# Performance work log

Hardware: AMD Instinct MI355X
Metric: run time of the kernel (lower is better)

Reference implementation:

```python
import jax, jax.numpy as jnp
import numpy as np

B, S, F = 16, 128, 64          # batch, seq_len, feature_dim
H = 256                        # hidden_dim
HEADS = 4
DH = H // HEADS                # GAT per-head dim = 64
AH = (2 * H) // HEADS          # temporal-attn head dim = 128
N = 1024                       # num graph nodes (edge_index.max()+1)
E = 16384                      # num edges (avg degree 16)
D2 = 2 * H                     # bi-LSTM output dim = 512
BN_INV = 1.0 / np.sqrt(1.0 + 1e-5)   # eval-mode BatchNorm1d (running mean=0, var=1)


def lstm_dir(x_sf, Wih, Whh, bih, bhh):
    # x_sf: [S, B, F]; torch gate order i, f, g, o
    h0 = jnp.zeros((x_sf.shape[1], Whh.shape[1]), x_sf.dtype)
    def step(carry, xt):
        h, c = carry
        z = xt @ Wih.T + h @ Whh.T + bih + bhh
        i, f, g, o = jnp.split(z, 4, axis=-1)
        c = jax.nn.sigmoid(f) * c + jax.nn.sigmoid(i) * jnp.tanh(g)
        h = jax.nn.sigmoid(o) * jnp.tanh(c)
        return (h, c), h
    _, hs = jax.lax.scan(step, (h0, h0), x_sf)
    return hs


def setup_inputs():
    key = jax.random.key(0)
    ks = jax.random.split(key, 32)
    g = lambda i, sh: jax.random.normal(ks[i], sh, jnp.float32) * 0.05
    return {
        "x": jax.random.normal(ks[0], (B, S, F), jnp.float32),
        "edge_index": jax.random.randint(ks[1], (2, E), 0, N),
        "Wih_f": g(2, (4 * H, F)), "Whh_f": g(3, (4 * H, H)),
        "bih_f": g(4, (4 * H,)), "bhh_f": g(5, (4 * H,)),
        "Wih_b": g(6, (4 * H, F)), "Whh_b": g(7, (4 * H, H)),
        "bih_b": g(8, (4 * H,)), "bhh_b": g(9, (4 * H,)),
        "Wq": g(10, (D2, D2)), "bq": g(11, (D2,)),
        "Wk": g(12, (D2, D2)), "bk": g(13, (D2,)),
        "Wv": g(14, (D2, D2)), "bv": g(15, (D2,)),
        "Wo": g(16, (D2, D2)), "bo": g(17, (D2,)),
        "W1": g(18, (D2, H)), "a1s": g(19, (HEADS, DH)), "a1d": g(20, (HEADS, DH)), "b1": g(21, (H,)),
        "g1": jnp.ones((H,), jnp.float32), "be1": jnp.zeros((H,), jnp.float32),
        "W2": g(22, (H, H)), "a2s": g(23, (HEADS, DH)), "a2d": g(24, (HEADS, DH)), "b2": g(25, (H,)),
        "g2": jnp.ones((H,), jnp.float32), "be2": jnp.zeros((H,), jnp.float32),
        "Wf": g(26, (H, 3 * H)), "bf": g(27, (H,)),
        "ln_g": jnp.ones((H,), jnp.float32), "ln_b": jnp.zeros((H,), jnp.float32),
    }


def reference(x, edge_index, Wih_f, Whh_f, bih_f, bhh_f, Wih_b, Whh_b, bih_b, bhh_b,
              Wq, bq, Wk, bk, Wv, bv, Wo, bo,
              W1, a1s, a1d, b1, g1, be1, W2, a2s, a2d, b2, g2, be2,
              Wf, bf, ln_g, ln_b):
    # ---- bidirectional LSTM ----
    xs = jnp.swapaxes(x, 0, 1)                                   # [S,B,F]
    hf = lstm_dir(xs, Wih_f, Whh_f, bih_f, bhh_f)
    hb = jnp.flip(lstm_dir(jnp.flip(xs, 0), Wih_b, Whh_b, bih_b, bhh_b), 0)
    t = jnp.swapaxes(jnp.concatenate([hf, hb], -1), 0, 1)        # [B,S,2H]
    # ---- temporal multi-head attention ----
    def proj(W, b):
        return (t @ W.T + b).reshape(B, S, HEADS, AH).transpose(0, 2, 1, 3)
    Q, K, V = proj(Wq, bq), proj(Wk, bk), proj(Wv, bv)
    scores = jnp.einsum('bhqd,bhkd->bhqk', Q, K) / np.sqrt(AH)
    attn = jax.nn.softmax(scores, -1)                            # [B,HEADS,S,S]
    ao = jnp.einsum('bhqk,bhkd->bhqd', attn, V).transpose(0, 2, 1, 3).reshape(B, S, D2)
    last = (ao @ Wo.T + bo)[:, -1, :]                            # [B,2H]
    # ---- 2-layer GAT per sample (PyG GATConv, add_self_loops=True), vmapped over batch ----
    loops = jnp.arange(N)
    src = jnp.concatenate([edge_index[0], loops])
    dst = jnp.concatenate([edge_index[1], loops])
    def gat(h_in, W, a_s, a_d, b):
        h = (h_in @ W).reshape(N, HEADS, DH)
        e = jax.nn.leaky_relu((h * a_s).sum(-1)[src] + (h * a_d).sum(-1)[dst], 0.2)  # [Etot,HEADS]
        m = jax.ops.segment_max(e, dst, num_segments=N)
        w = jnp.exp(e - m[dst])
        z = jax.ops.segment_sum(w, dst, num_segments=N)
        alpha = w / (z[dst] + 1e-16)
        out = jax.ops.segment_sum(alpha[:, :, None] * h[src], dst, num_segments=N)
        return out.reshape(N, H) + b
    def spatial(v):
        feat = jnp.broadcast_to(v, (N, D2))                      # uniform node features, per original
        h1 = jax.nn.elu(gat(feat, W1, a1s, a1d, b1) * BN_INV * g1 + be1)
        h2 = jax.nn.elu(gat(h1, W2, a2s, a2d, b2) * BN_INV * g2 + be2)
        return h2.mean(0)
    sp = jax.vmap(spatial)(last)                                 # [B,H]
    # ---- fusion: Linear + LayerNorm + ReLU (dropout = eval no-op) ----
    f = jnp.concatenate([last, sp], -1) @ Wf.T + bf
    mu = f.mean(-1, keepdims=True)
    var = ((f - mu) ** 2).mean(-1, keepdims=True)
    fused = jax.nn.relu((f - mu) / jnp.sqrt(var + 1e-5) * ln_g + ln_b)
    return fused, attn
```

## Files before the change

### kernel.cpp

```cpp
#include <hip/hip_runtime.h>


typedef unsigned short u16;
typedef unsigned int u32;
typedef __bf16 bf16x8 __attribute__((ext_vector_type(8)));
typedef float f32x4 __attribute__((ext_vector_type(4)));
typedef unsigned short ushort8v __attribute__((ext_vector_type(8)));
typedef unsigned int uint4v __attribute__((ext_vector_type(4)));

#define BN_INV_F 0.9999950000374997f
#define POISON 0xFFFFFFFFu

__device__ __forceinline__ float b2f(u16 u) {
  union { float f; unsigned int i; } v;
  v.i = ((unsigned int)u) << 16;
  return v.f;
}
__device__ __forceinline__ u16 f2b(float f) {
  union { float f; unsigned int i; } v;
  v.f = f;
  unsigned int x = v.i;
  unsigned int r = (x + 0x7FFFu + ((x >> 16) & 1u)) >> 16;
  return (u16)r;
}
__device__ __forceinline__ f32x4 mfma16(ushort8v a, ushort8v b, f32x4 c) {
  return __builtin_amdgcn_mfma_f32_16x16x32_bf16(
      __builtin_bit_cast(bf16x8, a), __builtin_bit_cast(bf16x8, b), c, 0, 0, 0);
}
__device__ __forceinline__ float sigm(float x) { return 1.f / (1.f + __expf(-x)); }
__device__ __forceinline__ float tanh_f(float x) {
  float e = __expf(2.f * x);
  return 1.f - 2.f / (e + 1.f);
}

__global__ __launch_bounds__(256) void lstm_kernel(
    const float* __restrict__ x,
    const float* __restrict__ Wih0, const float* __restrict__ Whh0,
    const float* __restrict__ bih0, const float* __restrict__ bhh0,
    const float* __restrict__ Wih1, const float* __restrict__ Whh1,
    const float* __restrict__ bih1, const float* __restrict__ bhh1,
    u32* __restrict__ hbuf,
    u16* __restrict__ tb)
{
  const int tid = threadIdx.x;
  const int bx = blockIdx.x;
  const int d = bx >> 4;
  const int q = bx & 15;
  const float* Wih = d ? Wih1 : Wih0;
  const float* Whh = d ? Whh1 : Whh0;
  const float* bih = d ? bih1 : bih0;
  const float* bhh = d ? bhh1 : bhh0;

  __shared__ u16 whh_s[64][264];
  __shared__ u16 wih_s[64][72];
  __shared__ u16 h_s[16][264];
  __shared__ u16 x_s[16][72];
  __shared__ float z_s[4][16][17];
  __shared__ float bias_s[64];

  {
    int r = tid >> 2, seg = tid & 3;
    int grow = ((r >> 4) << 8) + q * 16 + (r & 15);
    const float4* src = (const float4*)(Whh + grow * 256 + seg * 64);
#pragma unroll
    for (int i = 0; i < 16; i++) {
      float4 v = src[i];
      whh_s[r][seg * 64 + i * 4 + 0] = f2b(v.x);
      whh_s[r][seg * 64 + i * 4 + 1] = f2b(v.y);
      whh_s[r][seg * 64 + i * 4 + 2] = f2b(v.z);
      whh_s[r][seg * 64 + i * 4 + 3] = f2b(v.w);
    }
    const float4* src2 = (const float4*)(Wih + grow * 64 + seg * 16);
#pragma unroll
    for (int i = 0; i < 4; i++) {
      float4 v = src2[i];
      wih_s[r][seg * 16 + i * 4 + 0] = f2b(v.x);
      wih_s[r][seg * 16 + i * 4 + 1] = f2b(v.y);
      wih_s[r][seg * 16 + i * 4 + 2] = f2b(v.z);
      wih_s[r][seg * 16 + i * 4 + 3] = f2b(v.w);
    }
  }
  if (tid < 64) {
    int grow = ((tid >> 4) << 8) + q * 16 + (tid & 15);
    bias_s[tid] = bih[grow] + bhh[grow];
  }

  const int w = tid >> 6;
  const int ln = tid & 63;
  const int col16 = ln & 15;
  const int quad = ln >> 4;
  const int eb = tid >> 4;
  const int ec = tid & 15;
  float c_reg = 0.f;

  for (int t = 0; t < 128; t++) {
    const int pos = d ? (127 - t) : t;
    {
      int b_ = tid >> 4;
      int f0 = (tid & 15) * 4;
      float4 xv = *(const float4*)(x + (b_ * 128 + pos) * 64 + f0);
      x_s[b_][f0 + 0] = f2b(xv.x);
      x_s[b_][f0 + 1] = f2b(xv.y);
      x_s[b_][f0 + 2] = f2b(xv.z);
      x_s[b_][f0 + 3] = f2b(xv.w);
    }
    if (t > 0) {
      const u32* hw = hbuf + (t * 2 + d) * 2048 + tid * 8;
      uint4v a, b;
      for (;;) {
        asm volatile(
            "global_load_dwordx4 %0, %2, off sc1\n\t"
            "global_load_dwordx4 %1, %3, off sc1\n\t"
            "s_waitcnt vmcnt(0)"
            : "=v"(a), "=v"(b)
            : "v"(hw), "v"(hw + 4)
            : "memory");
        bool ok = (a.x != POISON) & (a.y != POISON) & (a.z != POISON) &
                  (a.w != POISON) & (b.x != POISON) & (b.y != POISON) &
                  (b.z != POISON) & (b.w != POISON);
        if (ok) break;
      }
      int b_ = tid >> 4, c0 = (tid & 15) * 16;
      *(u32*)&h_s[b_][c0 + 0] = a.x;
      *(u32*)&h_s[b_][c0 + 2] = a.y;
      *(u32*)&h_s[b_][c0 + 4] = a.z;
      *(u32*)&h_s[b_][c0 + 6] = a.w;
      *(u32*)&h_s[b_][c0 + 8] = b.x;
      *(u32*)&h_s[b_][c0 + 10] = b.y;
      *(u32*)&h_s[b_][c0 + 12] = b.z;
      *(u32*)&h_s[b_][c0 + 14] = b.w;
    }
    __syncthreads();

    f32x4 acc = {0.f, 0.f, 0.f, 0.f};
#pragma unroll
    for (int kt = 0; kt < 2; kt++) {
      ushort8v av = *(const ushort8v*)&x_s[col16][kt * 32 + quad * 8];
      ushort8v bv = *(const ushort8v*)&wih_s[w * 16 + col16][kt * 32 + quad * 8];
      acc = mfma16(av, bv, acc);
    }
    if (t > 0) {
#pragma unroll
      for (int kt = 0; kt < 8; kt++) {
        ushort8v av = *(const ushort8v*)&h_s[col16][kt * 32 + quad * 8];
        ushort8v bv = *(const ushort8v*)&whh_s[w * 16 + col16][kt * 32 + quad * 8];
        acc = mfma16(av, bv, acc);
      }
    }
#pragma unroll
    for (int reg = 0; reg < 4; reg++)
      z_s[w][quad * 4 + reg][col16] = acc[reg];
    __syncthreads();

    float zi = z_s[0][eb][ec] + bias_s[ec];
    float zf = z_s[1][eb][ec] + bias_s[16 + ec];
    float zg = z_s[2][eb][ec] + bias_s[32 + ec];
    float zo = z_s[3][eb][ec] + bias_s[48 + ec];
    float si = sigm(zi), sf = sigm(zf), so = sigm(zo);
    float tg = tanh_f(zg);
    c_reg = sf * c_reg + si * tg;
    float hv = so * tanh_f(c_reg);
    u32 my = (u32)f2b(hv);
    u32 hi = __shfl_down((int)my, 1);
    if ((ec & 1) == 0) {
      u32 word = my | (hi << 16);
      *(u32*)&tb[(eb * 128 + pos) * 512 + d * 256 + q * 16 + ec] = word;
      if (t < 127) {
        u32* dst = hbuf + ((t + 1) * 2 + d) * 2048 + eb * 128 + (q * 16 + ec) / 2;
        __hip_atomic_store(dst, word, __ATOMIC_RELAXED,
                           __HIP_MEMORY_SCOPE_AGENT);
      }
    }
  }
}

__global__ __launch_bounds__(256) void qkv_kernel(
    const u16* __restrict__ tb,
    const float* __restrict__ Wq, const float* __restrict__ bq,
    const float* __restrict__ Wk, const float* __restrict__ bk,
    const float* __restrict__ Wv, const float* __restrict__ bv,
    u16* __restrict__ Qb, u16* __restrict__ Kb, u16* __restrict__ Vb)
{
  const int tid = threadIdx.x;
  const int bxm = blockIdx.x, byn = blockIdx.y, bz = blockIdx.z;
  const float* W = (bz == 0) ? Wq : ((bz == 1) ? Wk : Wv);
  const float* bias = (bz == 0) ? bq : ((bz == 1) ? bk : bv);
  u16* outp = (bz == 0) ? Qb : ((bz == 1) ? Kb : Vb);

  __shared__ u16 a_s[64][40];
  __shared__ u16 b_s[64][40];
  const int w = tid >> 6, ln = tid & 63, col16 = ln & 15, quad = ln >> 4;

  f32x4 acc[4];
#pragma unroll
  for (int n = 0; n < 4; n++) acc[n] = (f32x4){0.f, 0.f, 0.f, 0.f};

  for (int kt = 0; kt < 16; kt++) {
    int r = tid >> 2, seg = tid & 3;
    *(ushort8v*)&a_s[r][seg * 8] =
        *(const ushort8v*)(tb + (bxm * 64 + r) * 512 + kt * 32 + seg * 8);
    const float4* wsrc = (const float4*)(W + (byn * 64 + r) * 512 + kt * 32 + seg * 8);
    float4 w0 = wsrc[0], w1 = wsrc[1];
    b_s[r][seg * 8 + 0] = f2b(w0.x);
    b_s[r][seg * 8 + 1] = f2b(w0.y);
    b_s[r][seg * 8 + 2] = f2b(w0.z);
    b_s[r][seg * 8 + 3] = f2b(w0.w);
    b_s[r][seg * 8 + 4] = f2b(w1.x);
    b_s[r][seg * 8 + 5] = f2b(w1.y);
    b_s[r][seg * 8 + 6] = f2b(w1.z);
    b_s[r][seg * 8 + 7] = f2b(w1.w);
    __syncthreads();
    ushort8v av = *(const ushort8v*)&a_s[w * 16 + col16][quad * 8];
#pragma unroll
    for (int n = 0; n < 4; n++) {
      ushort8v bvv = *(const ushort8v*)&b_s[n * 16 + col16][quad * 8];
      acc[n] = mfma16(av, bvv, acc[n]);
    }
    __syncthreads();
  }
#pragma unroll
  for (int n = 0; n < 4; n++) {
    float bs = bias[byn * 64 + n * 16 + col16];
#pragma unroll
    for (int reg = 0; reg < 4; reg++) {
      int row = bxm * 64 + w * 16 + quad * 4 + reg;
      outp[row * 512 + byn * 64 + n * 16 + col16] = f2b(acc[n][reg] + bs);
    }
  }
}

__global__ __launch_bounds__(256) void attn_kernel(
    const u16* __restrict__ Qb, const u16* __restrict__ Kb,
    float* __restrict__ attn_out)
{
  const int b = blockIdx.x, h = blockIdx.y, half = blockIdx.z;
  const int tid = threadIdx.x;
  __shared__ __align__(16) char smem[52224];
  u16 (*q_s)[136] = (u16(*)[136])smem;
  u16 (*k_s)[136] = (u16(*)[136])(smem + 17408);
  float (*sc)[132] = (float(*)[132])smem;

  const int w = tid >> 6, ln = tid & 63, col16 = ln & 15, quad = ln >> 4;
  {
    int r = tid >> 2, seg = tid & 3;
    const u16* src = Qb + (b * 128 + half * 64 + r) * 512 + h * 128 + seg * 32;
#pragma unroll
    for (int i = 0; i < 4; i++)
      *(ushort8v*)&q_s[r][seg * 32 + i * 8] = *(const ushort8v*)(src + i * 8);
    int r2 = tid >> 1, sg = tid & 1;
    const u16* src2 = Kb + (b * 128 + r2) * 512 + h * 128 + sg * 64;
#pragma unroll
    for (int i = 0; i < 8; i++)
      *(ushort8v*)&k_s[r2][sg * 64 + i * 8] = *(const ushort8v*)(src2 + i * 8);
  }
  __syncthreads();

  f32x4 acc[8];
#pragma unroll
  for (int n = 0; n < 8; n++) acc[n] = (f32x4){0.f, 0.f, 0.f, 0.f};
#pragma unroll
  for (int kd = 0; kd < 4; kd++) {
    ushort8v av = *(const ushort8v*)&q_s[w * 16 + col16][kd * 32 + quad * 8];
#pragma unroll
    for (int n = 0; n < 8; n++) {
      ushort8v bvv = *(const ushort8v*)&k_s[n * 16 + col16][kd * 32 + quad * 8];
      acc[n] = mfma16(av, bvv, acc[n]);
    }
  }
  __syncthreads();
  const float scale = 0.08838834764831845f;
#pragma unroll
  for (int n = 0; n < 8; n++)
#pragma unroll
    for (int reg = 0; reg < 4; reg++)
      sc[w * 16 + quad * 4 + reg][n * 16 + col16] = acc[n][reg] * scale;
  __syncthreads();

  const int row = tid >> 2, p = tid & 3;
  float m = -1e30f;
  for (int c0 = 0; c0 < 32; c0++) m = fmaxf(m, sc[row][p * 32 + c0]);
  m = fmaxf(m, __shfl_xor(m, 1));
  m = fmaxf(m, __shfl_xor(m, 2));
  float s = 0.f;
  for (int c0 = 0; c0 < 32; c0++) {
    float e = __expf(sc[row][p * 32 + c0] - m);
    sc[row][p * 32 + c0] = e;
    s += e;
  }
  s += __shfl_xor(s, 1);
  s += __shfl_xor(s, 2);
  float inv = 1.f / s;
  float* orow = attn_out + ((b * 4 + h) * 128 + half * 64 + row) * 128 + p * 32;
  for (int c0 = 0; c0 < 32; c0++) orow[c0] = sc[row][p * 32 + c0] * inv;
}

__global__ __launch_bounds__(256) void tail_kernel(
    const float* __restrict__ attn, const u16* __restrict__ Vb,
    const float* __restrict__ Wo, const float* __restrict__ bo,
    const float* __restrict__ W1, const float* __restrict__ b1,
    const float* __restrict__ g1, const float* __restrict__ be1,
    const float* __restrict__ W2, const float* __restrict__ pb2,
    const float* __restrict__ g2, const float* __restrict__ be2,
    const float* __restrict__ Wf, const float* __restrict__ bfv,
    const float* __restrict__ ln_g, const float* __restrict__ ln_b,
    float* __restrict__ dout)
{
  const int b = blockIdx.x, tid = threadIdx.x;
  __shared__ float arow[4][128];
  __shared__ float ao_s[512];
  __shared__ float last_s[512];
  __shared__ float h_s2[256];
  __shared__ float red_s[4];

#pragma unroll
  for (int e = 0; e < 2; e++) {
    int idx = tid + e * 256;
    int h = idx >> 7, k = idx & 127;
    arow[h][k] = attn[((b * 4 + h) * 128 + 127) * 128 + k];
  }
  __syncthreads();
#pragma unroll
  for (int pass = 0; pass < 2; pass++) {
    int d2 = tid + pass * 256;
    int hh = d2 >> 7;
    float acc = 0.f;
    for (int k = 0; k < 128; k++)
      acc += arow[hh][k] * b2f(Vb[(b * 128 + k) * 512 + d2]);
    ao_s[d2] = acc;
  }
  __syncthreads();
#pragma unroll
  for (int pass = 0; pass < 2; pass++) {
    int j = tid + pass * 256;
    float acc = bo[j];
    const float4* Wo4 = (const float4*)(Wo + j * 512);
    for (int k4 = 0; k4 < 128; k4++) {
      float4 wv = Wo4[k4];
      acc += ao_s[k4 * 4 + 0] * wv.x + ao_s[k4 * 4 + 1] * wv.y +
             ao_s[k4 * 4 + 2] * wv.z + ao_s[k4 * 4 + 3] * wv.w;
    }
    last_s[j] = acc;
  }
  __syncthreads();

  const int j = tid;
  float acc = 0.f;
  for (int k = 0; k < 512; k++) acc += last_s[k] * W1[k * 256 + j];
  float u = (acc + b1[j]) * BN_INV_F * g1[j] + be1[j];
  float h1 = u > 0.f ? u : expm1f(u);
  h_s2[j] = h1;
  __syncthreads();

  float acc2 = 0.f;
  for (int k = 0; k < 256; k++) acc2 += h_s2[k] * W2[k * 256 + j];
  float u2 = (acc2 + pb2[j]) * BN_INV_F * g2[j] + be2[j];
  float sp = u2 > 0.f ? u2 : expm1f(u2);
  __syncthreads();
  h_s2[j] = sp;
  __syncthreads();

  float f = bfv[j];
  const float4* Wf4 = (const float4*)(Wf + j * 768);
  for (int k4 = 0; k4 < 128; k4++) {
    float4 wv = Wf4[k4];
    f += last_s[k4 * 4 + 0] * wv.x + last_s[k4 * 4 + 1] * wv.y +
         last_s[k4 * 4 + 2] * wv.z + last_s[k4 * 4 + 3] * wv.w;
  }
  for (int k4 = 0; k4 < 64; k4++) {
    float4 wv = Wf4[128 + k4];
    f += h_s2[k4 * 4 + 0] * wv.x + h_s2[k4 * 4 + 1] * wv.y +
         h_s2[k4 * 4 + 2] * wv.z + h_s2[k4 * 4 + 3] * wv.w;
  }

  float v = f;
#pragma unroll
  for (int o = 32; o > 0; o >>= 1) v += __shfl_xor(v, o);
  if ((tid & 63) == 0) red_s[tid >> 6] = v;
  __syncthreads();
  float mu = (red_s[0] + red_s[1] + red_s[2] + red_s[3]) * (1.f / 256.f);
  float dv = f - mu;
  float vv = dv * dv;
#pragma unroll
  for (int o = 32; o > 0; o >>= 1) vv += __shfl_xor(vv, o);
  __syncthreads();
  if ((tid & 63) == 0) red_s[tid >> 6] = vv;
  __syncthreads();
  float var = (red_s[0] + red_s[1] + red_s[2] + red_s[3]) * (1.f / 256.f);
  float y = dv * rsqrtf(var + 1e-5f) * ln_g[j] + ln_b[j];
  dout[b * 256 + j] = fmaxf(y, 0.f);
}

extern "C" void kernel_launch(void* const* d_in, const int* in_sizes, int n_in,
                              void* d_out, int out_size, void* d_ws, size_t ws_size,
                              hipStream_t stream) {
  (void)in_sizes; (void)n_in; (void)out_size; (void)ws_size;
  const float* x     = (const float*)d_in[0];
  const float* Wih_f = (const float*)d_in[2];
  const float* Whh_f = (const float*)d_in[3];
  const float* bih_f = (const float*)d_in[4];
  const float* bhh_f = (const float*)d_in[5];
  const float* Wih_b = (const float*)d_in[6];
  const float* Whh_b = (const float*)d_in[7];
  const float* bih_b = (const float*)d_in[8];
  const float* bhh_b = (const float*)d_in[9];
  const float* Wq = (const float*)d_in[10]; const float* bq = (const float*)d_in[11];
  const float* Wk = (const float*)d_in[12]; const float* bk = (const float*)d_in[13];
  const float* Wv = (const float*)d_in[14]; const float* bv = (const float*)d_in[15];
  const float* Wo = (const float*)d_in[16]; const float* bo = (const float*)d_in[17];
  const float* W1 = (const float*)d_in[18];
  const float* b1 = (const float*)d_in[21];
  const float* g1 = (const float*)d_in[22]; const float* be1 = (const float*)d_in[23];
  const float* W2 = (const float*)d_in[24];
  const float* pb2 = (const float*)d_in[27];
  const float* g2 = (const float*)d_in[28]; const float* be2 = (const float*)d_in[29];
  const float* Wf = (const float*)d_in[30]; const float* bfv = (const float*)d_in[31];
  const float* ln_g = (const float*)d_in[32]; const float* ln_b = (const float*)d_in[33];

  float* dout = (float*)d_out;
  char* ws = (char*)d_ws;
  u32* hbuf = (u32*)(ws + 0);
  u16* tb   = (u16*)(ws + 2129920);
  u16* Qb   = (u16*)(ws + 4227072);
  u16* Kb   = (u16*)(ws + 6324224);
  u16* Vb   = (u16*)(ws + 8421376);

  (void)hipMemsetAsync(ws, 0xFF, 2097152, stream);
  lstm_kernel<<<32, 256, 0, stream>>>(x, Wih_f, Whh_f, bih_f, bhh_f,
                                      Wih_b, Whh_b, bih_b, bhh_b,
                                      hbuf, tb);
  qkv_kernel<<<dim3(32, 8, 3), 256, 0, stream>>>(tb, Wq, bq, Wk, bk, Wv, bv,
                                                 Qb, Kb, Vb);
  attn_kernel<<<dim3(16, 4, 2), 256, 0, stream>>>(Qb, Kb, dout + 4096);
  tail_kernel<<<16, 256, 0, stream>>>(dout + 4096, Vb, Wo, bo,
                                      W1, b1, g1, be1, W2, pb2, g2, be2,
                                      Wf, bfv, ln_g, ln_b, dout);
}
```

Baseline: 439.6 us.

## Shrink LSTM block to one wavefront, removing per-step barriers and LDS staging

The recurrent LSTM kernel now runs each block as a single 64-lane wavefront that computes all four gate tiles itself. The hidden state is loaded straight into MFMA operand registers and x is packed in registers, so the LDS staging and both per-step __syncthreads disappear from the serial critical path. Separately, the Q/K/V weights are converted to bf16 once by a new kernel, so the QKV GEMM loads bf16 directly. The risk is that each wave now issues four times as many MFMAs serially per step, plus one extra kernel launch.

```diff
diff --git a/kernel.cpp b/kernel.cpp
--- a/kernel.cpp
+++ b/kernel.cpp
@@ -23,6 +23,12 @@
   unsigned int r = (x + 0x7FFFu + ((x >> 16) & 1u)) >> 16;
   return (u16)r;
 }
+__device__ __forceinline__ ushort8v pack8(float4 a, float4 b) {
+  ushort8v v;
+  v[0] = f2b(a.x); v[1] = f2b(a.y); v[2] = f2b(a.z); v[3] = f2b(a.w);
+  v[4] = f2b(b.x); v[5] = f2b(b.y); v[6] = f2b(b.z); v[7] = f2b(b.w);
+  return v;
+}
 __device__ __forceinline__ f32x4 mfma16(ushort8v a, ushort8v b, f32x4 c) {
   return __builtin_amdgcn_mfma_f32_16x16x32_bf16(
       __builtin_bit_cast(bf16x8, a), __builtin_bit_cast(bf16x8, b), c, 0, 0, 0);
@@ -33,19 +39,18 @@
   return 1.f - 2.f / (e + 1.f);
 }
 
-__global__ __launch_bounds__(256) void lstm_kernel(
+__global__ __launch_bounds__(64) void lstm_kernel(
     const float* __restrict__ x,
     const float* __restrict__ Wih0, const float* __restrict__ Whh0,
     const float* __restrict__ bih0, const float* __restrict__ bhh0,
     const float* __restrict__ Wih1, const float* __restrict__ Whh1,
     const float* __restrict__ bih1, const float* __restrict__ bhh1,
     u32* __restrict__ hbuf,
-    u16* __restrict__ tb)
+    u32* __restrict__ tb32)
 {
-  const int tid = threadIdx.x;
+  const int ln = threadIdx.x;
   const int bx = blockIdx.x;
-  const int d = bx >> 4;
-  const int q = bx & 15;
+  const int d = bx >> 4, q = bx & 15;
   const float* Wih = d ? Wih1 : Wih0;
   const float* Whh = d ? Whh1 : Whh0;
   const float* bih = d ? bih1 : bih0;
@@ -53,137 +58,146 @@
 
   __shared__ u16 whh_s[64][264];
   __shared__ u16 wih_s[64][72];
-  __shared__ u16 h_s[16][264];
-  __shared__ u16 x_s[16][72];
-  __shared__ float z_s[4][16][17];
-  __shared__ float bias_s[64];
+
+  const int i15 = ln & 15;
+  const int quad = ln >> 4;
 
   {
-    int r = tid >> 2, seg = tid & 3;
-    int grow = ((r >> 4) << 8) + q * 16 + (r & 15);
-    const float4* src = (const float4*)(Whh + grow * 256 + seg * 64);
-#pragma unroll
-    for (int i = 0; i < 16; i++) {
-      float4 v = src[i];
-      whh_s[r][seg * 64 + i * 4 + 0] = f2b(v.x);
-      whh_s[r][seg * 64 + i * 4 + 1] = f2b(v.y);
-      whh_s[r][seg * 64 + i * 4 + 2] = f2b(v.z);
-      whh_s[r][seg * 64 + i * 4 + 3] = f2b(v.w);
-    }
-    const float4* src2 = (const float4*)(Wih + grow * 64 + seg * 16);
-#pragma unroll
-    for (int i = 0; i < 4; i++) {
-      float4 v = src2[i];
-      wih_s[r][seg * 16 + i * 4 + 0] = f2b(v.x);
-      wih_s[r][seg * 16 + i * 4 + 1] = f2b(v.y);
-      wih_s[r][seg * 16 + i * 4 + 2] = f2b(v.z);
-      wih_s[r][seg * 16 + i * 4 + 3] = f2b(v.w);
-    }
-  }
-  if (tid < 64) {
-    int grow = ((tid >> 4) << 8) + q * 16 + (tid & 15);
-    bias_s[tid] = bih[grow] + bhh[grow];
-  }
-
-  const int w = tid >> 6;
-  const int ln = tid & 63;
-  const int col16 = ln & 15;
-  const int quad = ln >> 4;
-  const int eb = tid >> 4;
-  const int ec = tid & 15;
-  float c_reg = 0.f;
+    int grow = ((ln >> 4) << 8) + q * 16 + (ln & 15);
+    const float4* src = (const float4*)(Whh + grow * 256);
+#pragma unroll 4
+    for (int c = 0; c < 32; c++)
+      *(ushort8v*)&whh_s[ln][c * 8] = pack8(src[2 * c], src[2 * c + 1]);
+    const float4* s2 = (const float4*)(Wih + grow * 64);
+#pragma unroll
+    for (int c = 0; c < 8; c++)
+      *(ushort8v*)&wih_s[ln][c * 8] = pack8(s2[2 * c], s2[2 * c + 1]);
+  }
+  float bias4[4];
+#pragma unroll
+  for (int g = 0; g < 4; g++) {
+    int grow = (g << 8) + q * 16 + i15;
+    bias4[g] = bih[grow] + bhh[grow];
+  }
+  __syncthreads();
+
+  float c_r[4] = {0.f, 0.f, 0.f, 0.f};
 
   for (int t = 0; t < 128; t++) {
     const int pos = d ? (127 - t) : t;
-    {
-      int b_ = tid >> 4;
-      int f0 = (tid & 15) * 4;
-      float4 xv = *(const float4*)(x + (b_ * 128 + pos) * 64 + f0);
-      x_s[b_][f0 + 0] = f2b(xv.x);
-      x_s[b_][f0 + 1] = f2b(xv.y);
-      x_s[b_][f0 + 2] = f2b(xv.z);
-      x_s[b_][f0 + 3] = f2b(xv.w);
-    }
+
+    const float4* xp = (const float4*)(x + (i15 * 128 + pos) * 64);
+    float4 xa0 = xp[quad * 2], xa1 = xp[quad * 2 + 1];
+    float4 xb0 = xp[8 + quad * 2], xb1 = xp[9 + quad * 2];
+
+    uint4v p0, p1, p2, p3, p4, p5, p6, p7;
     if (t > 0) {
-      const u32* hw = hbuf + (t * 2 + d) * 2048 + tid * 8;
-      uint4v a, b;
+      const u32* hw = hbuf + ((t * 2 + d) << 11) + (i15 << 7) + (quad << 2);
       for (;;) {
         asm volatile(
-            "global_load_dwordx4 %0, %2, off sc1\n\t"
-            "global_load_dwordx4 %1, %3, off sc1\n\t"
+            "global_load_dwordx4 %0, %8, off sc1\n\t"
+            "global_load_dwordx4 %1, %9, off sc1\n\t"
+            "global_load_dwordx4 %2, %10, off sc1\n\t"
+            "global_load_dwordx4 %3, %11, off sc1\n\t"
+            "global_load_dwordx4 %4, %12, off sc1\n\t"
+            "global_load_dwordx4 %5, %13, off sc1\n\t"
+            "global_load_dwordx4 %6, %14, off sc1\n\t"
+            "global_load_dwordx4 %7, %15, off sc1\n\t"
             "s_waitcnt vmcnt(0)"
-            : "=v"(a), "=v"(b)
-            : "v"(hw), "v"(hw + 4)
+            : "=v"(p0), "=v"(p1), "=v"(p2), "=v"(p3),
+              "=v"(p4), "=v"(p5), "=v"(p6), "=v"(p7)
+            : "v"(hw), "v"(hw + 16), "v"(hw + 32), "v"(hw + 48),
+              "v"(hw + 64), "v"(hw + 80), "v"(hw + 96), "v"(hw + 112)
             : "memory");
-        bool ok = (a.x != POISON) & (a.y != POISON) & (a.z != POISON) &
-                  (a.w != POISON) & (b.x != POISON) & (b.y != POISON) &
-                  (b.z != POISON) & (b.w != POISON);
-        if (ok) break;
+        bool ok = (p0.x != POISON) & (p0.y != POISON) & (p0.z != POISON) & (p0.w != POISON) &
+                  (p1.x != POISON) & (p1.y != POISON) & (p1.z != POISON) & (p1.w != POISON) &
+                  (p2.x != POISON) & (p2.y != POISON) & (p2.z != POISON) & (p2.w != POISON) &
+                  (p3.x != POISON) & (p3.y != POISON) & (p3.z != POISON) & (p3.w != POISON) &
+                  (p4.x != POISON) & (p4.y != POISON) & (p4.z != POISON) & (p4.w != POISON) &
+                  (p5.x != POISON) & (p5.y != POISON) & (p5.z != POISON) & (p5.w != POISON) &
+                  (p6.x != POISON) & (p6.y != POISON) & (p6.z != POISON) & (p6.w != POISON) &
+                  (p7.x != POISON) & (p7.y != POISON) & (p7.z != POISON) & (p7.w != POISON);
+        if (__ballot(ok) == ~0ull) break;
       }
-      int b_ = tid >> 4, c0 = (tid & 15) * 16;
-      *(u32*)&h_s[b_][c0 + 0] = a.x;
-      *(u32*)&h_s[b_][c0 + 2] = a.y;
-      *(u32*)&h_s[b_][c0 + 4] = a.z;
-      *(u32*)&h_s[b_][c0 + 6] = a.w;
-      *(u32*)&h_s[b_][c0 + 8] = b.x;
-      *(u32*)&h_s[b_][c0 + 10] = b.y;
-      *(u32*)&h_s[b_][c0 + 12] = b.z;
-      *(u32*)&h_s[b_][c0 + 14] = b.w;
-    }
-    __syncthreads();
-
-    f32x4 acc = {0.f, 0.f, 0.f, 0.f};
-#pragma unroll
-    for (int kt = 0; kt < 2; kt++) {
-      ushort8v av = *(const ushort8v*)&x_s[col16][kt * 32 + quad * 8];
-      ushort8v bv = *(const ushort8v*)&wih_s[w * 16 + col16][kt * 32 + quad * 8];
-      acc = mfma16(av, bv, acc);
+    }
+
+    f32x4 acc[4];
+#pragma unroll
+    for (int n = 0; n < 4; n++) acc[n] = (f32x4){0.f, 0.f, 0.f, 0.f};
+    ushort8v xf0 = pack8(xa0, xa1), xf1 = pack8(xb0, xb1);
+#pragma unroll
+    for (int n = 0; n < 4; n++) {
+      acc[n] = mfma16(xf0, *(const ushort8v*)&wih_s[n * 16 + i15][quad * 8], acc[n]);
+      acc[n] = mfma16(xf1, *(const ushort8v*)&wih_s[n * 16 + i15][32 + quad * 8], acc[n]);
     }
     if (t > 0) {
-#pragma unroll
-      for (int kt = 0; kt < 8; kt++) {
-        ushort8v av = *(const ushort8v*)&h_s[col16][kt * 32 + quad * 8];
-        ushort8v bv = *(const ushort8v*)&whh_s[w * 16 + col16][kt * 32 + quad * 8];
-        acc = mfma16(av, bv, acc);
+      ushort8v af[8] = {
+          __builtin_bit_cast(ushort8v, p0), __builtin_bit_cast(ushort8v, p1),
+          __builtin_bit_cast(ushort8v, p2), __builtin_bit_cast(ushort8v, p3),
+          __builtin_bit_cast(ushort8v, p4), __builtin_bit_cast(ushort8v, p5),
+          __builtin_bit_cast(ushort8v, p6), __builtin_bit_cast(ushort8v, p7)};
+#pragma unroll
+      for (int kt = 0; kt < 8; kt++)
+#pragma unroll
+        for (int n = 0; n < 4; n++)
+          acc[n] = mfma16(af[kt],
+                          *(const ushort8v*)&whh_s[n * 16 + i15][kt * 32 + quad * 8],
+                          acc[n]);
+    }
+
+    u32 word[4];
+#pragma unroll
+    for (int r = 0; r < 4; r++) {
+      float zi = acc[0][r] + bias4[0];
+      float zf = acc[1][r] + bias4[1];
+      float zg = acc[2][r] + bias4[2];
+      float zo = acc[3][r] + bias4[3];
+      float si = sigm(zi), sf = sigm(zf), so = sigm(zo);
+      float tg = tanh_f(zg);
+      c_r[r] = sf * c_r[r] + si * tg;
+      float hv = so * tanh_f(c_r[r]);
+      u32 m = (u32)f2b(hv);
+      u32 o = (u32)__shfl_xor((int)m, 1);
+      word[r] = m | (o << 16);
+    }
+    if (!(i15 & 1)) {
+      const int cw = q * 8 + (i15 >> 1);
+      if (t < 127) {
+        u32* hb = hbuf + (((t + 1) * 2 + d) << 11) + cw;
+#pragma unroll
+        for (int r = 0; r < 4; r++)
+          __hip_atomic_store(hb + (quad * 4 + r) * 128, word[r],
+                             __ATOMIC_RELAXED, __HIP_MEMORY_SCOPE_AGENT);
       }
-    }
-#pragma unroll
-    for (int reg = 0; reg < 4; reg++)
-      z_s[w][quad * 4 + reg][col16] = acc[reg];
-    __syncthreads();
-
-    float zi = z_s[0][eb][ec] + bias_s[ec];
-    float zf = z_s[1][eb][ec] + bias_s[16 + ec];
-    float zg = z_s[2][eb][ec] + bias_s[32 + ec];
-    float zo = z_s[3][eb][ec] + bias_s[48 + ec];
-    float si = sigm(zi), sf = sigm(zf), so = sigm(zo);
-    float tg = tanh_f(zg);
-    c_reg = sf * c_reg + si * tg;
-    float hv = so * tanh_f(c_reg);
-    u32 my = (u32)f2b(hv);
-    u32 hi = __shfl_down((int)my, 1);
-    if ((ec & 1) == 0) {
-      u32 word = my | (hi << 16);
-      *(u32*)&tb[(eb * 128 + pos) * 512 + d * 256 + q * 16 + ec] = word;
-      if (t < 127) {
-        u32* dst = hbuf + ((t + 1) * 2 + d) * 2048 + eb * 128 + (q * 16 + ec) / 2;
-        __hip_atomic_store(dst, word, __ATOMIC_RELAXED,
-                           __HIP_MEMORY_SCOPE_AGENT);
-      }
-    }
-  }
+#pragma unroll
+      for (int r = 0; r < 4; r++)
+        tb32[((quad * 4 + r) * 128 + pos) * 256 + d * 128 + cw] = word[r];
+    }
+  }
+}
+
+__global__ __launch_bounds__(256) void wcvt_kernel(
+    const float* __restrict__ Wq, const float* __restrict__ Wk,
+    const float* __restrict__ Wv,
+    u16* __restrict__ oq, u16* __restrict__ ok2, u16* __restrict__ ov)
+{
+  const float* s = (blockIdx.y == 0) ? Wq : ((blockIdx.y == 1) ? Wk : Wv);
+  u16* o = (blockIdx.y == 0) ? oq : ((blockIdx.y == 1) ? ok2 : ov);
+  int idx = blockIdx.x * 256 + threadIdx.x;
+  const float4* sp = (const float4*)s + idx * 2;
+  *(ushort8v*)(o + idx * 8) = pack8(sp[0], sp[1]);
 }
 
 __global__ __launch_bounds__(256) void qkv_kernel(
     const u16* __restrict__ tb,
-    const float* __restrict__ Wq, const float* __restrict__ bq,
-    const float* __restrict__ Wk, const float* __restrict__ bk,
-    const float* __restrict__ Wv, const float* __restrict__ bv,
+    const u16* __restrict__ Wqb, const float* __restrict__ bq,
+    const u16* __restrict__ Wkb, const float* __restrict__ bk,
+    const u16* __restrict__ Wvb, const float* __restrict__ bv,
     u16* __restrict__ Qb, u16* __restrict__ Kb, u16* __restrict__ Vb)
 {
   const int tid = threadIdx.x;
   const int bxm = blockIdx.x, byn = blockIdx.y, bz = blockIdx.z;
-  const float* W = (bz == 0) ? Wq : ((bz == 1) ? Wk : Wv);
+  const u16* W = (bz == 0) ? Wqb : ((bz == 1) ? Wkb : Wvb);
   const float* bias = (bz == 0) ? bq : ((bz == 1) ? bk : bv);
   u16* outp = (bz == 0) ? Qb : ((bz == 1) ? Kb : Vb);
 
@@ -199,16 +213,8 @@
     int r = tid >> 2, seg = tid & 3;
     *(ushort8v*)&a_s[r][seg * 8] =
         *(const ushort8v*)(tb + (bxm * 64 + r) * 512 + kt * 32 + seg * 8);
-    const float4* wsrc = (const float4*)(W + (byn * 64 + r) * 512 + kt * 32 + seg * 8);
-    float4 w0 = wsrc[0], w1 = wsrc[1];
-    b_s[r][seg * 8 + 0] = f2b(w0.x);
-    b_s[r][seg * 8 + 1] = f2b(w0.y);
-    b_s[r][seg * 8 + 2] = f2b(w0.z);
-    b_s[r][seg * 8 + 3] = f2b(w0.w);
-    b_s[r][seg * 8 + 4] = f2b(w1.x);
-    b_s[r][seg * 8 + 5] = f2b(w1.y);
-    b_s[r][seg * 8 + 6] = f2b(w1.z);
-    b_s[r][seg * 8 + 7] = f2b(w1.w);
+    *(ushort8v*)&b_s[r][seg * 8] =
+        *(const ushort8v*)(W + (byn * 64 + r) * 512 + kt * 32 + seg * 8);
     __syncthreads();
     ushort8v av = *(const ushort8v*)&a_s[w * 16 + col16][quad * 8];
 #pragma unroll
@@ -419,16 +425,20 @@
   float* dout = (float*)d_out;
   char* ws = (char*)d_ws;
   u32* hbuf = (u32*)(ws + 0);
-  u16* tb   = (u16*)(ws + 2129920);
-  u16* Qb   = (u16*)(ws + 4227072);
-  u16* Kb   = (u16*)(ws + 6324224);
-  u16* Vb   = (u16*)(ws + 8421376);
+  u16* tb   = (u16*)(ws + 2097152);
+  u16* Qb   = (u16*)(ws + 4194304);
+  u16* Kb   = (u16*)(ws + 6291456);
+  u16* Vb   = (u16*)(ws + 8388608);
+  u16* Wqb  = (u16*)(ws + 10485760);
+  u16* Wkb  = (u16*)(ws + 11010048);
+  u16* Wvb  = (u16*)(ws + 11534336);
 
   (void)hipMemsetAsync(ws, 0xFF, 2097152, stream);
-  lstm_kernel<<<32, 256, 0, stream>>>(x, Wih_f, Whh_f, bih_f, bhh_f,
-                                      Wih_b, Whh_b, bih_b, bhh_b,
-                                      hbuf, tb);
-  qkv_kernel<<<dim3(32, 8, 3), 256, 0, stream>>>(tb, Wq, bq, Wk, bk, Wv, bv,
+  lstm_kernel<<<32, 64, 0, stream>>>(x, Wih_f, Whh_f, bih_f, bhh_f,
+                                     Wih_b, Whh_b, bih_b, bhh_b,
+                                     hbuf, (u32*)tb);
+  wcvt_kernel<<<dim3(128, 3), 256, 0, stream>>>(Wq, Wk, Wv, Wqb, Wkb, Wvb);
+  qkv_kernel<<<dim3(32, 8, 3), 256, 0, stream>>>(tb, Wqb, bq, Wkb, bk, Wvb, bv,
                                                  Qb, Kb, Vb);
   attn_kernel<<<dim3(16, 4, 2), 256, 0, stream>>>(Qb, Kb, dout + 4096);
   tail_kernel<<<16, 256, 0, stream>>>(dout + 4096, Vb, Wo, bo,
```

New measurement: 624.8 us. 42.1% more time.

## Drop full V projection via associativity; pre-convert Wq/Wk to bf16 in spare LSTM blocks

Applied to the files above, without the earlier changes.

The tail kernel only needs the last query row's attention output, so it computes attn_row·tb first and then multiplies by Wv. This removes the full V projection GEMM, and the QKV GEMM becomes a QK-only GEMM. Extra blocks in the LSTM launch convert Wq/Wk to bf16 once, so the GEMM loads bf16 tiles directly, and the LSTM weight staging uses packed 8-wide stores. The risk is that the tail kernel now does a serial 512x512 fp32 matvec per head inside only 16 blocks.

```diff
diff --git a/kernel.cpp b/kernel.cpp
--- a/kernel.cpp
+++ b/kernel.cpp
@@ -23,6 +23,12 @@
   unsigned int r = (x + 0x7FFFu + ((x >> 16) & 1u)) >> 16;
   return (u16)r;
 }
+__device__ __forceinline__ ushort8v pack8(float4 a, float4 b) {
+  ushort8v v;
+  v[0] = f2b(a.x); v[1] = f2b(a.y); v[2] = f2b(a.z); v[3] = f2b(a.w);
+  v[4] = f2b(b.x); v[5] = f2b(b.y); v[6] = f2b(b.z); v[7] = f2b(b.w);
+  return v;
+}
 __device__ __forceinline__ f32x4 mfma16(ushort8v a, ushort8v b, f32x4 c) {
   return __builtin_amdgcn_mfma_f32_16x16x32_bf16(
       __builtin_bit_cast(bf16x8, a), __builtin_bit_cast(bf16x8, b), c, 0, 0, 0);
@@ -39,11 +45,27 @@
     const float* __restrict__ bih0, const float* __restrict__ bhh0,
     const float* __restrict__ Wih1, const float* __restrict__ Whh1,
     const float* __restrict__ bih1, const float* __restrict__ bhh1,
+    const float* __restrict__ Wq, const float* __restrict__ Wk,
+    u16* __restrict__ Wqb, u16* __restrict__ Wkb,
     u32* __restrict__ hbuf,
     u16* __restrict__ tb)
 {
   const int tid = threadIdx.x;
   const int bx = blockIdx.x;
+
+  if (bx >= 32) {
+    const float* s = (bx < 48) ? Wq : Wk;
+    u16* o = (bx < 48) ? Wqb : Wkb;
+    int idx = ((bx & 15) << 8) + tid;
+#pragma unroll
+    for (int i = 0; i < 8; i++) {
+      int e8 = i * 4096 + idx;
+      const float4* sp = (const float4*)s + e8 * 2;
+      *(ushort8v*)(o + e8 * 8) = pack8(sp[0], sp[1]);
+    }
+    return;
+  }
+
   const int d = bx >> 4;
   const int q = bx & 15;
   const float* Wih = d ? Wih1 : Wih0;
@@ -63,22 +85,11 @@
     int grow = ((r >> 4) << 8) + q * 16 + (r & 15);
     const float4* src = (const float4*)(Whh + grow * 256 + seg * 64);
 #pragma unroll
-    for (int i = 0; i < 16; i++) {
-      float4 v = src[i];
-      whh_s[r][seg * 64 + i * 4 + 0] = f2b(v.x);
-      whh_s[r][seg * 64 + i * 4 + 1] = f2b(v.y);
-      whh_s[r][seg * 64 + i * 4 + 2] = f2b(v.z);
-      whh_s[r][seg * 64 + i * 4 + 3] = f2b(v.w);
-    }
+    for (int i = 0; i < 8; i++)
+      *(ushort8v*)&whh_s[r][seg * 64 + i * 8] = pack8(src[2 * i], src[2 * i + 1]);
     const float4* src2 = (const float4*)(Wih + grow * 64 + seg * 16);
-#pragma unroll
-    for (int i = 0; i < 4; i++) {
-      float4 v = src2[i];
-      wih_s[r][seg * 16 + i * 4 + 0] = f2b(v.x);
-      wih_s[r][seg * 16 + i * 4 + 1] = f2b(v.y);
-      wih_s[r][seg * 16 + i * 4 + 2] = f2b(v.z);
-      wih_s[r][seg * 16 + i * 4 + 3] = f2b(v.w);
-    }
+    *(ushort8v*)&wih_s[r][seg * 16] = pack8(src2[0], src2[1]);
+    *(ushort8v*)&wih_s[r][seg * 16 + 8] = pack8(src2[2], src2[3]);
   }
   if (tid < 64) {
     int grow = ((tid >> 4) << 8) + q * 16 + (tid & 15);
@@ -162,7 +173,7 @@
     float hv = so * tanh_f(c_reg);
     u32 my = (u32)f2b(hv);
     u32 hi = __shfl_down((int)my, 1);
-    if ((ec & 1) == 0) {
+    if (!(ec & 1)) {
       u32 word = my | (hi << 16);
       *(u32*)&tb[(eb * 128 + pos) * 512 + d * 256 + q * 16 + ec] = word;
       if (t < 127) {
@@ -174,18 +185,17 @@
   }
 }
 
-__global__ __launch_bounds__(256) void qkv_kernel(
+__global__ __launch_bounds__(256) void qk_kernel(
     const u16* __restrict__ tb,
-    const float* __restrict__ Wq, const float* __restrict__ bq,
-    const float* __restrict__ Wk, const float* __restrict__ bk,
-    const float* __restrict__ Wv, const float* __restrict__ bv,
-    u16* __restrict__ Qb, u16* __restrict__ Kb, u16* __restrict__ Vb)
+    const u16* __restrict__ Wqb, const float* __restrict__ bq,
+    const u16* __restrict__ Wkb, const float* __restrict__ bk,
+    u16* __restrict__ Qb, u16* __restrict__ Kb)
 {
   const int tid = threadIdx.x;
   const int bxm = blockIdx.x, byn = blockIdx.y, bz = blockIdx.z;
-  const float* W = (bz == 0) ? Wq : ((bz == 1) ? Wk : Wv);
-  const float* bias = (bz == 0) ? bq : ((bz == 1) ? bk : bv);
-  u16* outp = (bz == 0) ? Qb : ((bz == 1) ? Kb : Vb);
+  const u16* W = (bz == 0) ? Wqb : Wkb;
+  const float* bias = (bz == 0) ? bq : bk;
+  u16* outp = (bz == 0) ? Qb : Kb;
 
   __shared__ u16 a_s[64][40];
   __shared__ u16 b_s[64][40];
@@ -199,16 +209,8 @@
     int r = tid >> 2, seg = tid & 3;
     *(ushort8v*)&a_s[r][seg * 8] =
         *(const ushort8v*)(tb + (bxm * 64 + r) * 512 + kt * 32 + seg * 8);
-    const float4* wsrc = (const float4*)(W + (byn * 64 + r) * 512 + kt * 32 + seg * 8);
-    float4 w0 = wsrc[0], w1 = wsrc[1];
-    b_s[r][seg * 8 + 0] = f2b(w0.x);
-    b_s[r][seg * 8 + 1] = f2b(w0.y);
-    b_s[r][seg * 8 + 2] = f2b(w0.z);
-    b_s[r][seg * 8 + 3] = f2b(w0.w);
-    b_s[r][seg * 8 + 4] = f2b(w1.x);
-    b_s[r][seg * 8 + 5] = f2b(w1.y);
-    b_s[r][seg * 8 + 6] = f2b(w1.z);
-    b_s[r][seg * 8 + 7] = f2b(w1.w);
+    *(ushort8v*)&b_s[r][seg * 8] =
+        *(const ushort8v*)(W + (byn * 64 + r) * 512 + kt * 32 + seg * 8);
     __syncthreads();
     ushort8v av = *(const ushort8v*)&a_s[w * 16 + col16][quad * 8];
 #pragma unroll
@@ -295,7 +297,8 @@
 }
 
 __global__ __launch_bounds__(256) void tail_kernel(
-    const float* __restrict__ attn, const u16* __restrict__ Vb,
+    const float* __restrict__ attn, const u16* __restrict__ tb,
+    const float* __restrict__ Wv, const float* __restrict__ bv,
     const float* __restrict__ Wo, const float* __restrict__ bo,
     const float* __restrict__ W1, const float* __restrict__ b1,
     const float* __restrict__ g1, const float* __restrict__ be1,
@@ -307,6 +310,7 @@
 {
   const int b = blockIdx.x, tid = threadIdx.x;
   __shared__ float arow[4][128];
+  __shared__ float u_s[4][512];
   __shared__ float ao_s[512];
   __shared__ float last_s[512];
   __shared__ float h_s2[256];
@@ -319,16 +323,36 @@
     arow[h][k] = attn[((b * 4 + h) * 128 + 127) * 128 + k];
   }
   __syncthreads();
+
+  {
+    int h = tid >> 6, c0 = (tid & 63) * 8;
+    float acc8[8] = {0.f};
+    for (int k = 0; k < 128; k++) {
+      float a = arow[h][k];
+      ushort8v tv = *(const ushort8v*)(tb + (b * 128 + k) * 512 + c0);
+#pragma unroll
+      for (int i = 0; i < 8; i++) acc8[i] += a * b2f(tv[i]);
+    }
+#pragma unroll
+    for (int i = 0; i < 8; i++) u_s[h][c0 + i] = acc8[i];
+  }
+  __syncthreads();
+
 #pragma unroll
   for (int pass = 0; pass < 2; pass++) {
-    int d2 = tid + pass * 256;
-    int hh = d2 >> 7;
-    float acc = 0.f;
-    for (int k = 0; k < 128; k++)
-      acc += arow[hh][k] * b2f(Vb[(b * 128 + k) * 512 + d2]);
-    ao_s[d2] = acc;
-  }
-  __syncthreads();
+    int col = tid + pass * 256;
+    int h = col >> 7;
+    float acc = bv[col];
+    const float4* Wv4 = (const float4*)(Wv + col * 512);
+    for (int k4 = 0; k4 < 128; k4++) {
+      float4 wv = Wv4[k4];
+      acc += u_s[h][k4 * 4 + 0] * wv.x + u_s[h][k4 * 4 + 1] * wv.y +
+             u_s[h][k4 * 4 + 2] * wv.z + u_s[h][k4 * 4 + 3] * wv.w;
+    }
+    ao_s[col] = acc;
+  }
+  __syncthreads();
+
 #pragma unroll
   for (int pass = 0; pass < 2; pass++) {
     int j = tid + pass * 256;
@@ -419,19 +443,19 @@
   float* dout = (float*)d_out;
   char* ws = (char*)d_ws;
   u32* hbuf = (u32*)(ws + 0);
-  u16* tb   = (u16*)(ws + 2129920);
-  u16* Qb   = (u16*)(ws + 4227072);
-  u16* Kb   = (u16*)(ws + 6324224);
-  u16* Vb   = (u16*)(ws + 8421376);
+  u16* tb   = (u16*)(ws + 2097152);
+  u16* Qb   = (u16*)(ws + 4194304);
+  u16* Kb   = (u16*)(ws + 6291456);
+  u16* Wqb  = (u16*)(ws + 8388608);
+  u16* Wkb  = (u16*)(ws + 8912896);
 
   (void)hipMemsetAsync(ws, 0xFF, 2097152, stream);
-  lstm_kernel<<<32, 256, 0, stream>>>(x, Wih_f, Whh_f, bih_f, bhh_f,
+  lstm_kernel<<<64, 256, 0, stream>>>(x, Wih_f, Whh_f, bih_f, bhh_f,
                                       Wih_b, Whh_b, bih_b, bhh_b,
-                                      hbuf, tb);
-  qkv_kernel<<<dim3(32, 8, 3), 256, 0, stream>>>(tb, Wq, bq, Wk, bk, Wv, bv,
-                                                 Qb, Kb, Vb);
+                                      Wq, Wk, Wqb, Wkb, hbuf, tb);
+  qk_kernel<<<dim3(32, 8, 2), 256, 0, stream>>>(tb, Wqb, bq, Wkb, bk, Qb, Kb);
   attn_kernel<<<dim3(16, 4, 2), 256, 0, stream>>>(Qb, Kb, dout + 4096);
-  tail_kernel<<<16, 256, 0, stream>>>(dout + 4096, Vb, Wo, bo,
+  tail_kernel<<<16, 256, 0, stream>>>(dout + 4096, tb, Wv, bv, Wo, bo,
                                       W1, b1, g1, be1, W2, pb2, g2, be2,
                                       Wf, bfv, ln_g, ln_b, dout);
 }
```

Measured after the change: 457.0 us. 1.04x slower.
